# Kernel optimization log

Measured on AMD Instinct MI355X. Metric: run time of the kernel, lower is better.

Reference implementation:

```python
import jax, jax.numpy as jnp
import numpy as np

RADIUS = 50
HEADS = 4
BN_EPS = 1e-5


def setup_inputs() -> dict:
    key = jax.random.key(0)
    B, C, L = 2, 256, 1536
    D = C // HEADS
    ks = jax.random.split(key, 8)
    s = 0.05  # weight init scale
    return {
        "x": jax.random.normal(ks[0], (B, C, L), jnp.float32),
        "Wc": jax.random.normal(ks[1], (C, C), jnp.float32) * s,
        "bc": jnp.zeros((C,), jnp.float32),
        "Wq": jax.random.normal(ks[2], (C, C), jnp.float32) * s,
        "bq": jnp.zeros((C,), jnp.float32),
        "Wk": jax.random.normal(ks[3], (C, C), jnp.float32) * s,
        "bk": jnp.zeros((C,), jnp.float32),
        "emb": jax.random.normal(ks[4], (2 * RADIUS + 1, D), jnp.float32) * s,
        "Wf": jax.random.normal(ks[5], (C, C), jnp.float32) * s,
        "bf": jnp.zeros((C,), jnp.float32),
        "gamma": jnp.ones((C,), jnp.float32),
        "beta": jnp.zeros((C,), jnp.float32),
        "scale": jnp.full((C,), 0.1, jnp.float32),
    }


def reference(x, Wc, bc, Wq, bq, Wk, bk, emb, Wf, bf, gamma, beta, scale):
    B, C, L = x.shape
    H = HEADS
    D = C // H
    R = RADIUS

    def conv1x1(W, b, y):  # 1x1 Conv1d == per-position matmul
        return jnp.einsum('oc,bcl->bol', W, y) + b[None, :, None]

    def split(y):  # [B,C,L] -> [B,H,D,L]
        return y.reshape(B, H, D, L)

    content = split(conv1x1(Wc, bc, x))
    query = split(conv1x1(Wq, bq, x))
    key_ = split(conv1x1(Wk, bk, x))

    steps = jnp.arange(L)
    relative = steps[:, None] - steps[None, :]                 # [L,L]
    rel_clamped = jnp.clip(relative, -R, R)
    embs = emb[R + rel_clamped]                                # [L,L,D] gather

    dots = jnp.einsum('bhct,bhcs->bhts', query, key_)          # [B,H,L,L]
    dots = dots + 0.3 * jnp.einsum('bhct,tsc->bhts', query, embs)
    dots = jnp.where(jnp.abs(relative) <= R, dots, -jnp.inf)   # band mask

    weights = jax.nn.softmax(dots, axis=-1)                    # [B,H,L,L]

    out = jnp.einsum('bhts,bhcs->bhct', weights, content)      # [B,H,D,L]
    out = out + 0.3 * jnp.einsum('bhts,tsc->bhct', weights, embs)
    out = out.reshape(B, C, L)

    out = conv1x1(Wf, bf, out)
    # BatchNorm1d in training mode: batch stats over (B, L) per channel
    mean = out.mean(axis=(0, 2), keepdims=True)
    var = out.var(axis=(0, 2), keepdims=True)
    out = (out - mean) / jnp.sqrt(var + BN_EPS)
    out = out * gamma[None, :, None] + beta[None, :, None]
    return jax.nn.relu(out) * scale[None, :, None]
```

## Files before the change

### kernel.cpp

```cpp
#include <hip/hip_runtime.h>

typedef unsigned short u16;
typedef unsigned int u32;
typedef __bf16 bf16x8 __attribute__((ext_vector_type(8)));
typedef float f32x4 __attribute__((ext_vector_type(4)));

#define MFMA16 __builtin_amdgcn_mfma_f32_16x16x32_bf16

__device__ __forceinline__ u16 f2bf(float f) {
    u32 u = __float_as_uint(f);
    u32 r = (u + 0x7fffu + ((u >> 16) & 1u)) >> 16;
    return (u16)r;
}
__device__ __forceinline__ float bf2f(u16 h) {
    return __uint_as_float(((u32)h) << 16);
}
__device__ __forceinline__ bf16x8 ld8(const u16* p) {
    return *reinterpret_cast<const bf16x8*>(p);
}

__global__ __launch_bounds__(256) void prep(
    const float* __restrict__ x,
    const float* __restrict__ Wc, const float* __restrict__ Wq,
    const float* __restrict__ Wk, const float* __restrict__ Wf,
    const float* __restrict__ emb,
    u16* __restrict__ xT,
    u16* __restrict__ wcb, u16* __restrict__ wqb, u16* __restrict__ wkb,
    u16* __restrict__ wfb, u16* __restrict__ embR, u16* __restrict__ embT)
{
    const int tid = threadIdx.x;
    const int z = blockIdx.z;
    if (z < 2) {
        __shared__ u16 tile[64][65];
        const int b = z, c0 = blockIdx.y * 64, l0 = blockIdx.x * 64;
        const int cc = tid >> 2, lq = (tid & 3) * 16;
        const float* xp = x + (size_t)((b * 256 + c0 + cc) * 1536 + l0 + lq);
        #pragma unroll
        for (int i = 0; i < 4; ++i) {
            float4 v = *reinterpret_cast<const float4*>(xp + i * 4);
            tile[cc][lq + i * 4 + 0] = f2bf(v.x);
            tile[cc][lq + i * 4 + 1] = f2bf(v.y);
            tile[cc][lq + i * 4 + 2] = f2bf(v.z);
            tile[cc][lq + i * 4 + 3] = f2bf(v.w);
        }
        __syncthreads();
        const int ll = tid >> 2, cq = (tid & 3) * 16;
        u16* op = xT + (size_t)((b * 1536 + l0 + ll) * 256 + c0 + cq);
        #pragma unroll
        for (int i = 0; i < 16; ++i) op[i] = tile[cq + i][ll];
    } else {
        const int idx0 = (blockIdx.y * 24 + blockIdx.x) * 256 + tid;
        for (int i = idx0; i < 65536; i += 24576) {
            wcb[i] = f2bf(Wc[i]); wqb[i] = f2bf(Wq[i]);
            wkb[i] = f2bf(Wk[i]); wfb[i] = f2bf(Wf[i]);
        }
        if (idx0 < 112 * 64) {
            const int j = idx0 >> 6, d = idx0 & 63;
            embR[idx0] = (j < 101) ? f2bf(0.3f * emb[(100 - j) * 64 + d]) : (u16)0;
        }
        if (idx0 < 64 * 128) {
            const int d = idx0 >> 7, j = idx0 & 127;
            embT[idx0] = (j < 101) ? f2bf(0.3f * emb[(100 - j) * 64 + d]) : (u16)0;
        }
    }
}

__global__ __launch_bounds__(128) void gemm_qkc(
    const u16* __restrict__ xT,
    const u16* __restrict__ Wq, const float* __restrict__ bq,
    const u16* __restrict__ Wk, const float* __restrict__ bk,
    const u16* __restrict__ Wc, const float* __restrict__ bc,
    u16* __restrict__ qo, u16* __restrict__ ko, u16* __restrict__ co)
{
    const int tid = threadIdx.x, wv = tid >> 6, lane = tid & 63;
    const int l15 = lane & 15, kg8 = (lane >> 4) * 8;
    const int z = blockIdx.z, b = z & 1, which = z >> 1;
    const u16* W = (which == 0) ? Wq : (which == 1) ? Wk : Wc;
    const float* bias = (which == 0) ? bq : (which == 1) ? bk : bc;
    const int l0 = blockIdx.x * 64 + wv * 32;
    const int ch0 = blockIdx.y * 32;
    const u16* xp = xT + (size_t)(b * 1536 + l0 + l15) * 256 + kg8;
    const u16* wp = W + (size_t)(ch0 + l15) * 256 + kg8;
    const u16* ap = (which == 2) ? wp : xp;
    const u16* bp = (which == 2) ? xp : wp;

    bf16x8 a0r[8], a1r[8], b0r[8], b1r[8];
    #pragma unroll
    for (int kd = 0; kd < 8; ++kd) {
        a0r[kd] = ld8(ap + kd * 32);
        a1r[kd] = ld8(ap + 4096 + kd * 32);
        b0r[kd] = ld8(bp + kd * 32);
        b1r[kd] = ld8(bp + 4096 + kd * 32);
    }
    const f32x4 zf = {0.f, 0.f, 0.f, 0.f};
    f32x4 acc[2][2] = {{zf, zf}, {zf, zf}};
    #pragma unroll
    for (int kd = 0; kd < 8; ++kd) {
        acc[0][0] = MFMA16(a0r[kd], b0r[kd], acc[0][0], 0, 0, 0);
        acc[0][1] = MFMA16(a0r[kd], b1r[kd], acc[0][1], 0, 0, 0);
        acc[1][0] = MFMA16(a1r[kd], b0r[kd], acc[1][0], 0, 0, 0);
        acc[1][1] = MFMA16(a1r[kd], b1r[kd], acc[1][1], 0, 0, 0);
    }
    if (which < 2) {
        u16* outp = which ? ko : qo;
        float bv[2];
        bv[0] = bias[ch0 + l15];
        bv[1] = bias[ch0 + 16 + l15];
        #pragma unroll
        for (int mf = 0; mf < 2; ++mf)
            #pragma unroll
            for (int nf = 0; nf < 2; ++nf)
                #pragma unroll
                for (int r = 0; r < 4; ++r) {
                    const int row = l0 + mf * 16 + (lane >> 4) * 4 + r;
                    outp[(size_t)(b * 1536 + row) * 256 + ch0 + nf * 16 + l15] =
                        f2bf(acc[mf][nf][r] + bv[nf]);
                }
    } else {
        #pragma unroll
        for (int mf = 0; mf < 2; ++mf)
            #pragma unroll
            for (int r = 0; r < 4; ++r) {
                const int ch = ch0 + mf * 16 + (lane >> 4) * 4 + r;
                const float bv = bias[ch];
                #pragma unroll
                for (int nf = 0; nf < 2; ++nf)
                    co[(size_t)(b * 256 + ch) * 1536 + l0 + nf * 16 + l15] =
                        f2bf(acc[mf][nf][r] + bv);
            }
    }
}

__global__ __launch_bounds__(128) void gemm_f(
    const u16* __restrict__ W, const float* __restrict__ bias,
    const u16* __restrict__ srcT, u16* __restrict__ outp)
{
    const int tid = threadIdx.x, wv = tid >> 6, lane = tid & 63;
    const int l15 = lane & 15, kg8 = (lane >> 4) * 8;
    const int b = blockIdx.z;
    const int l0 = blockIdx.x * 64 + wv * 32;
    const int ch0 = blockIdx.y * 32;
    const u16* ap = W + (size_t)(ch0 + l15) * 256 + kg8;
    const u16* bp = srcT + (size_t)(b * 1536 + l0 + l15) * 256 + kg8;

    bf16x8 a0r[8], a1r[8], b0r[8], b1r[8];
    #pragma unroll
    for (int kd = 0; kd < 8; ++kd) {
        a0r[kd] = ld8(ap + kd * 32);
        a1r[kd] = ld8(ap + 4096 + kd * 32);
        b0r[kd] = ld8(bp + kd * 32);
        b1r[kd] = ld8(bp + 4096 + kd * 32);
    }
    const f32x4 zf = {0.f, 0.f, 0.f, 0.f};
    f32x4 acc[2][2] = {{zf, zf}, {zf, zf}};
    #pragma unroll
    for (int kd = 0; kd < 8; ++kd) {
        acc[0][0] = MFMA16(a0r[kd], b0r[kd], acc[0][0], 0, 0, 0);
        acc[0][1] = MFMA16(a0r[kd], b1r[kd], acc[0][1], 0, 0, 0);
        acc[1][0] = MFMA16(a1r[kd], b0r[kd], acc[1][0], 0, 0, 0);
        acc[1][1] = MFMA16(a1r[kd], b1r[kd], acc[1][1], 0, 0, 0);
    }
    #pragma unroll
    for (int mf = 0; mf < 2; ++mf)
        #pragma unroll
        for (int r = 0; r < 4; ++r) {
            const int ch = ch0 + mf * 16 + (lane >> 4) * 4 + r;
            const float bv = bias[ch];
            #pragma unroll
            for (int nf = 0; nf < 2; ++nf)
                outp[(size_t)(b * 256 + ch) * 1536 + l0 + nf * 16 + l15] =
                    f2bf(acc[mf][nf][r] + bv);
        }
}

#define WST 168
#define WBST 136
#define BST 114

__global__ __launch_bounds__(128) void attn_mfma(
    const u16* __restrict__ q, const u16* __restrict__ k,
    const u16* __restrict__ cont, const u16* __restrict__ embR,
    const u16* __restrict__ embT, u16* __restrict__ outp)
{
    __shared__ u16 wls[2][16][WST];
    __shared__ u16 wbs[2][16][WBST];
    __shared__ u16 bss[2][16][BST];
    const int tid = threadIdx.x;
    const int wv = tid >> 6, lane = tid & 63;
    const int l15 = lane & 15, kg8 = (lane >> 4) * 8;
    const int tt0 = (blockIdx.x * 2 + wv) * 16;
    const int bh = blockIdx.y, b = bh >> 2, h = bh & 3;
    u16* wl = &wls[wv][0][0];
    u16* wb = &wbs[wv][0][0];
    u16* bs = &bss[wv][0][0];

    const u16* qp = q + (size_t)(b * 1536 + tt0 + l15) * 256 + h * 64 + kg8;
    const bf16x8 a0 = ld8(qp);
    const bf16x8 a1 = ld8(qp + 32);
    bf16x8 k0r[9], k1r[9];
    #pragma unroll
    for (int nf = 0; nf < 9; ++nf) {
        int s = tt0 - 64 + nf * 16 + l15;
        int sc = s < 0 ? 0 : (s > 1535 ? 1535 : s);
        const u16* kp = k + (size_t)(b * 1536 + sc) * 256 + h * 64 + kg8;
        k0r[nf] = ld8(kp);
        k1r[nf] = ld8(kp + 32);
    }

    for (int i = lane; i < 16 * 8; i += 64) {
        const int t = i >> 3, c = 144 + ((i & 7) << 1);
        *reinterpret_cast<u32*>(&wl[t * WST + c]) = 0;
    }
    for (int i = lane; i < 16 * 27; i += 64) {
        const int t = i / 27, j = 101 + (i - t * 27);
        wb[t * WBST + j] = 0;
    }

    const f32x4 zf = {0.f, 0.f, 0.f, 0.f};
    f32x4 dacc[9];
    f32x4 eacc[7];
    #pragma unroll
    for (int i = 0; i < 9; ++i) dacc[i] = zf;
    #pragma unroll
    for (int i = 0; i < 7; ++i) eacc[i] = zf;

    #pragma unroll
    for (int nf = 0; nf < 9; ++nf) {
        dacc[nf] = MFMA16(a0, k0r[nf], dacc[nf], 0, 0, 0);
        dacc[nf] = MFMA16(a1, k1r[nf], dacc[nf], 0, 0, 0);
    }
    #pragma unroll
    for (int jf = 0; jf < 7; ++jf) {
        const u16* ep = embR + (jf * 16 + l15) * 64 + kg8;
        eacc[jf] = MFMA16(a0, ld8(ep), eacc[jf], 0, 0, 0);
        eacc[jf] = MFMA16(a1, ld8(ep + 32), eacc[jf], 0, 0, 0);
    }
    #pragma unroll
    for (int jf = 0; jf < 7; ++jf)
        #pragma unroll
        for (int r = 0; r < 4; ++r) {
            const int t = (lane >> 4) * 4 + r;
            bs[t * BST + jf * 16 + l15] = f2bf(eacc[jf][r]);
        }
    #pragma unroll
    for (int nf = 0; nf < 9; ++nf)
        #pragma unroll
        for (int r = 0; r < 4; ++r) {
            const int t = (lane >> 4) * 4 + r;
            const int cs = nf * 16 + l15;
            const int j = cs - t - 14;
            const int s = tt0 - 64 + cs;
            float v = dacc[nf][r];
            if (j >= 0 && j < 101 && s >= 0 && s < 1536)
                v += bf2f(bs[t * BST + j]);
            else
                v = -1e30f;
            dacc[nf][r] = v;
        }
    float inv[4];
    #pragma unroll
    for (int r = 0; r < 4; ++r) {
        float m = dacc[0][r];
        #pragma unroll
        for (int nf = 1; nf < 9; ++nf) m = fmaxf(m, dacc[nf][r]);
        m = fmaxf(m, __shfl_xor(m, 1));
        m = fmaxf(m, __shfl_xor(m, 2));
        m = fmaxf(m, __shfl_xor(m, 4));
        m = fmaxf(m, __shfl_xor(m, 8));
        float ss = 0.f;
        #pragma unroll
        for (int nf = 0; nf < 9; ++nf) {
            float e = __expf(dacc[nf][r] - m);
            dacc[nf][r] = e;
            ss += e;
        }
        ss += __shfl_xor(ss, 1);
        ss += __shfl_xor(ss, 2);
        ss += __shfl_xor(ss, 4);
        ss += __shfl_xor(ss, 8);
        inv[r] = 1.f / ss;
    }
    #pragma unroll
    for (int nf = 0; nf < 9; ++nf)
        #pragma unroll
        for (int r = 0; r < 4; ++r) {
            const int t = (lane >> 4) * 4 + r;
            const int cs = nf * 16 + l15;
            const u16 w16 = f2bf(dacc[nf][r] * inv[r]);
            wl[t * WST + cs] = w16;
            const int j = cs - t - 14;
            if (j >= 0 && j < 101) wb[t * WBST + j] = w16;
        }

    f32x4 oacc[4];
    #pragma unroll
    for (int i = 0; i < 4; ++i) oacc[i] = zf;
    #pragma unroll
    for (int kf = 0; kf < 5; ++kf) {
        const bf16x8 aw = ld8(&wl[l15 * WST + kf * 32 + kg8]);
        int sb = tt0 - 64 + kf * 32 + kg8;
        int sbc = sb < 0 ? 0 : (sb > 1528 ? 1528 : sb);
        #pragma unroll
        for (int nf = 0; nf < 4; ++nf) {
            const u16* cp = cont + (size_t)(b * 256 + h * 64 + nf * 16 + l15) * 1536 + sbc;
            oacc[nf] = MFMA16(aw, ld8(cp), oacc[nf], 0, 0, 0);
        }
    }
    #pragma unroll
    for (int kf = 0; kf < 4; ++kf) {
        const bf16x8 ab = ld8(&wb[l15 * WBST + kf * 32 + kg8]);
        #pragma unroll
        for (int nf = 0; nf < 4; ++nf) {
            const u16* ep = embT + (nf * 16 + l15) * 128 + kf * 32 + kg8;
            oacc[nf] = MFMA16(ab, ld8(ep), oacc[nf], 0, 0, 0);
        }
    }
    #pragma unroll
    for (int nf = 0; nf < 4; ++nf)
        #pragma unroll
        for (int r = 0; r < 4; ++r) {
            const int t = (lane >> 4) * 4 + r;
            outp[(size_t)(b * 1536 + tt0 + t) * 256 + h * 64 + nf * 16 + l15] =
                f2bf(oacc[nf][r]);
        }
}

__global__ __launch_bounds__(256) void bn_apply(
    const u16* __restrict__ pre, const float* __restrict__ gamma,
    const float* __restrict__ beta, const float* __restrict__ scale,
    float* __restrict__ out)
{
    const int o = blockIdx.x;
    const int tid = threadIdx.x;
    float v[12];
    float sum = 0.f, sumsq = 0.f;
    #pragma unroll
    for (int g = 0; g < 6; ++g) {
        const int b = (g >= 3);
        const int l = (g - 3 * b) * 512 + tid * 2;
        const u32 w = *reinterpret_cast<const u32*>(&pre[(size_t)(b * 256 + o) * 1536 + l]);
        const float v0 = __uint_as_float(w << 16);
        const float v1 = __uint_as_float(w & 0xffff0000u);
        v[g * 2] = v0; v[g * 2 + 1] = v1;
        sum += v0 + v1;
        sumsq = fmaf(v0, v0, sumsq);
        sumsq = fmaf(v1, v1, sumsq);
    }
    #pragma unroll
    for (int off = 1; off < 64; off <<= 1) {
        sum += __shfl_xor(sum, off);
        sumsq += __shfl_xor(sumsq, off);
    }
    __shared__ float rs[4], rq[4];
    const int wave = tid >> 6;
    if ((tid & 63) == 0) { rs[wave] = sum; rq[wave] = sumsq; }
    __syncthreads();
    sum = rs[0] + rs[1] + rs[2] + rs[3];
    sumsq = rq[0] + rq[1] + rq[2] + rq[3];
    const float mean = sum * (1.f / 3072.f);
    const float var = sumsq * (1.f / 3072.f) - mean * mean;
    const float is = rsqrtf(var + 1e-5f);
    const float gm = gamma[o] * is;
    const float b2 = beta[o] - mean * gm;
    const float sc = scale[o];
    #pragma unroll
    for (int g = 0; g < 6; ++g) {
        const int b = (g >= 3);
        const int l = (g - 3 * b) * 512 + tid * 2;
        float2 o2;
        o2.x = fmaxf(fmaf(v[g * 2], gm, b2), 0.f) * sc;
        o2.y = fmaxf(fmaf(v[g * 2 + 1], gm, b2), 0.f) * sc;
        *reinterpret_cast<float2*>(&out[(size_t)(b * 256 + o) * 1536 + l]) = o2;
    }
}

extern "C" void kernel_launch(void* const* d_in, const int* in_sizes, int n_in,
                              void* d_out, int out_size, void* d_ws, size_t ws_size,
                              hipStream_t stream) {
    const float* x     = (const float*)d_in[0];
    const float* Wc    = (const float*)d_in[1];
    const float* bc    = (const float*)d_in[2];
    const float* Wq    = (const float*)d_in[3];
    const float* bq    = (const float*)d_in[4];
    const float* Wk    = (const float*)d_in[5];
    const float* bk    = (const float*)d_in[6];
    const float* emb   = (const float*)d_in[7];
    const float* Wf    = (const float*)d_in[8];
    const float* bf    = (const float*)d_in[9];
    const float* gamma = (const float*)d_in[10];
    const float* beta  = (const float*)d_in[11];
    const float* scale = (const float*)d_in[12];
    float* out = (float*)d_out;
    u16* ws = (u16*)d_ws;

    const size_t NLC = 786432;
    u16* xT   = ws;
    u16* qb   = ws + NLC;
    u16* kb   = ws + 2 * NLC;
    u16* cbuf = ws + 3 * NLC;
    u16* abuf = ws + 4 * NLC;
    u16* pbuf = ws + 5 * NLC;
    u16* wcb  = ws + 6 * NLC;
    u16* wqb  = wcb + 65536;
    u16* wkb  = wqb + 65536;
    u16* wfb  = wkb + 65536;
    u16* embR = wfb + 65536;
    u16* embT = embR + 112 * 64;

    prep<<<dim3(24, 4, 3), 256, 0, stream>>>(x, Wc, Wq, Wk, Wf, emb,
                                             xT, wcb, wqb, wkb, wfb, embR, embT);
    gemm_qkc<<<dim3(24, 8, 6), 128, 0, stream>>>(xT, wqb, bq, wkb, bk, wcb, bc,
                                                 qb, kb, cbuf);
    attn_mfma<<<dim3(48, 8), 128, 0, stream>>>(qb, kb, cbuf, embR, embT, abuf);
    gemm_f<<<dim3(24, 8, 2), 128, 0, stream>>>(wfb, bf, abuf, pbuf);
    bn_apply<<<256, 256, 0, stream>>>(pbuf, gamma, beta, scale, out);
}
```

Baseline: 118.0 us.

## Fuse all stages into one persistent kernel with flag-based grid barriers

Replaces the five separate launches (prep, QKC GEMM, banded attention, output GEMM, BatchNorm) with a single 256-block persistent kernel. The stages are separated by a software grid barrier built from per-block release/acquire flags in workspace memory. Work is remapped from grid dimensions to per-wave loop indices, and all stages share one shared-memory buffer. The aim is to remove launch overhead and inter-kernel gaps. In exchange it relies on all 256 blocks being co-resident, and the flags are never reset between calls, which risks the barrier not holding on repeated invocations.

```diff
diff --git a/kernel.cpp b/kernel.cpp
--- a/kernel.cpp
+++ b/kernel.cpp
@@ -6,6 +6,11 @@
 typedef float f32x4 __attribute__((ext_vector_type(4)));
 
 #define MFMA16 __builtin_amdgcn_mfma_f32_16x16x32_bf16
+#define NBLK 256
+#define WST 168
+#define WBST 136
+#define BST 114
+#define WCHUNK (16 * (WST + WBST + BST))
 
 __device__ __forceinline__ u16 f2bf(float f) {
     u32 u = __float_as_uint(f);
@@ -19,358 +24,363 @@
     return *reinterpret_cast<const bf16x8*>(p);
 }
 
-__global__ __launch_bounds__(256) void prep(
+__device__ __forceinline__ void gsync(u32* flags, int p) {
+    __syncthreads();
+    if (threadIdx.x == 0) {
+        __threadfence();
+        __hip_atomic_store(&flags[blockIdx.x], (u32)p, __ATOMIC_RELEASE,
+                           __HIP_MEMORY_SCOPE_AGENT);
+    }
+    while ((int)__hip_atomic_load(&flags[threadIdx.x], __ATOMIC_ACQUIRE,
+                                  __HIP_MEMORY_SCOPE_AGENT) < p) {
+        __builtin_amdgcn_s_sleep(2);
+    }
+    __threadfence();
+    __syncthreads();
+}
+
+__global__ __launch_bounds__(256, 1) void fused_all(
     const float* __restrict__ x,
-    const float* __restrict__ Wc, const float* __restrict__ Wq,
-    const float* __restrict__ Wk, const float* __restrict__ Wf,
+    const float* __restrict__ Wc, const float* __restrict__ bc,
+    const float* __restrict__ Wq, const float* __restrict__ bq,
+    const float* __restrict__ Wk, const float* __restrict__ bk,
     const float* __restrict__ emb,
+    const float* __restrict__ Wf, const float* __restrict__ bf,
+    const float* __restrict__ gamma, const float* __restrict__ beta,
+    const float* __restrict__ scale,
     u16* __restrict__ xT,
     u16* __restrict__ wcb, u16* __restrict__ wqb, u16* __restrict__ wkb,
-    u16* __restrict__ wfb, u16* __restrict__ embR, u16* __restrict__ embT)
+    u16* __restrict__ wfb, u16* __restrict__ embR, u16* __restrict__ embT,
+    u16* __restrict__ qb, u16* __restrict__ kb, u16* __restrict__ cbuf,
+    u16* __restrict__ abuf, u16* __restrict__ pbuf,
+    u32* __restrict__ flags,
+    float* __restrict__ out)
 {
+    __shared__ u32 smem32[13376];
+    u16* smem = (u16*)smem32;
     const int tid = threadIdx.x;
-    const int z = blockIdx.z;
-    if (z < 2) {
-        __shared__ u16 tile[64][65];
-        const int b = z, c0 = blockIdx.y * 64, l0 = blockIdx.x * 64;
+    const int blk = blockIdx.x;
+    const int wv = tid >> 6, lane = tid & 63;
+    const int l15 = lane & 15, kg8 = (lane >> 4) * 8;
+    const f32x4 zf = {0.f, 0.f, 0.f, 0.f};
+
+    if (blk < 192) {
+        const int b = blk / 96, c0 = ((blk / 24) & 3) * 64, l0 = (blk % 24) * 64;
+        u16* tile = smem;
         const int cc = tid >> 2, lq = (tid & 3) * 16;
         const float* xp = x + (size_t)((b * 256 + c0 + cc) * 1536 + l0 + lq);
         #pragma unroll
         for (int i = 0; i < 4; ++i) {
             float4 v = *reinterpret_cast<const float4*>(xp + i * 4);
-            tile[cc][lq + i * 4 + 0] = f2bf(v.x);
-            tile[cc][lq + i * 4 + 1] = f2bf(v.y);
-            tile[cc][lq + i * 4 + 2] = f2bf(v.z);
-            tile[cc][lq + i * 4 + 3] = f2bf(v.w);
+            tile[cc * 65 + lq + i * 4 + 0] = f2bf(v.x);
+            tile[cc * 65 + lq + i * 4 + 1] = f2bf(v.y);
+            tile[cc * 65 + lq + i * 4 + 2] = f2bf(v.z);
+            tile[cc * 65 + lq + i * 4 + 3] = f2bf(v.w);
         }
         __syncthreads();
         const int ll = tid >> 2, cq = (tid & 3) * 16;
         u16* op = xT + (size_t)((b * 1536 + l0 + ll) * 256 + c0 + cq);
         #pragma unroll
-        for (int i = 0; i < 16; ++i) op[i] = tile[cq + i][ll];
+        for (int i = 0; i < 16; ++i) op[i] = tile[(cq + i) * 65 + ll];
     } else {
-        const int idx0 = (blockIdx.y * 24 + blockIdx.x) * 256 + tid;
-        for (int i = idx0; i < 65536; i += 24576) {
+        const int g = (blk - 192) * 256 + tid;
+        #pragma unroll
+        for (int rep = 0; rep < 4; ++rep) {
+            const int i = g + rep * 16384;
             wcb[i] = f2bf(Wc[i]); wqb[i] = f2bf(Wq[i]);
             wkb[i] = f2bf(Wk[i]); wfb[i] = f2bf(Wf[i]);
         }
-        if (idx0 < 112 * 64) {
-            const int j = idx0 >> 6, d = idx0 & 63;
-            embR[idx0] = (j < 101) ? f2bf(0.3f * emb[(100 - j) * 64 + d]) : (u16)0;
-        }
-        if (idx0 < 64 * 128) {
-            const int d = idx0 >> 7, j = idx0 & 127;
-            embT[idx0] = (j < 101) ? f2bf(0.3f * emb[(100 - j) * 64 + d]) : (u16)0;
-        }
-    }
-}
-
-__global__ __launch_bounds__(128) void gemm_qkc(
-    const u16* __restrict__ xT,
-    const u16* __restrict__ Wq, const float* __restrict__ bq,
-    const u16* __restrict__ Wk, const float* __restrict__ bk,
-    const u16* __restrict__ Wc, const float* __restrict__ bc,
-    u16* __restrict__ qo, u16* __restrict__ ko, u16* __restrict__ co)
-{
-    const int tid = threadIdx.x, wv = tid >> 6, lane = tid & 63;
-    const int l15 = lane & 15, kg8 = (lane >> 4) * 8;
-    const int z = blockIdx.z, b = z & 1, which = z >> 1;
-    const u16* W = (which == 0) ? Wq : (which == 1) ? Wk : Wc;
-    const float* bias = (which == 0) ? bq : (which == 1) ? bk : bc;
-    const int l0 = blockIdx.x * 64 + wv * 32;
-    const int ch0 = blockIdx.y * 32;
-    const u16* xp = xT + (size_t)(b * 1536 + l0 + l15) * 256 + kg8;
-    const u16* wp = W + (size_t)(ch0 + l15) * 256 + kg8;
-    const u16* ap = (which == 2) ? wp : xp;
-    const u16* bp = (which == 2) ? xp : wp;
-
-    bf16x8 a0r[8], a1r[8], b0r[8], b1r[8];
-    #pragma unroll
-    for (int kd = 0; kd < 8; ++kd) {
-        a0r[kd] = ld8(ap + kd * 32);
-        a1r[kd] = ld8(ap + 4096 + kd * 32);
-        b0r[kd] = ld8(bp + kd * 32);
-        b1r[kd] = ld8(bp + 4096 + kd * 32);
-    }
-    const f32x4 zf = {0.f, 0.f, 0.f, 0.f};
-    f32x4 acc[2][2] = {{zf, zf}, {zf, zf}};
-    #pragma unroll
-    for (int kd = 0; kd < 8; ++kd) {
-        acc[0][0] = MFMA16(a0r[kd], b0r[kd], acc[0][0], 0, 0, 0);
-        acc[0][1] = MFMA16(a0r[kd], b1r[kd], acc[0][1], 0, 0, 0);
-        acc[1][0] = MFMA16(a1r[kd], b0r[kd], acc[1][0], 0, 0, 0);
-        acc[1][1] = MFMA16(a1r[kd], b1r[kd], acc[1][1], 0, 0, 0);
-    }
-    if (which < 2) {
-        u16* outp = which ? ko : qo;
-        float bv[2];
-        bv[0] = bias[ch0 + l15];
-        bv[1] = bias[ch0 + 16 + l15];
-        #pragma unroll
-        for (int mf = 0; mf < 2; ++mf)
-            #pragma unroll
-            for (int nf = 0; nf < 2; ++nf)
+        if (g < 112 * 64) {
+            const int j = g >> 6, d = g & 63;
+            embR[g] = (j < 101) ? f2bf(0.3f * emb[(100 - j) * 64 + d]) : (u16)0;
+        }
+        if (g < 64 * 128) {
+            const int d = g >> 7, j = g & 127;
+            embT[g] = (j < 101) ? f2bf(0.3f * emb[(100 - j) * 64 + d]) : (u16)0;
+        }
+    }
+    gsync(flags, 1);
+
+    for (int u = blk * 4 + wv; u < 2304; u += 1024) {
+        const int z = u / 384;
+        const int r = u - z * 384;
+        const int l0 = (r >> 3) * 32;
+        const int ch0 = (r & 7) * 32;
+        const int b = z & 1, which = z >> 1;
+        const u16* W = (which == 0) ? wqb : (which == 1) ? wkb : wcb;
+        const float* bias = (which == 0) ? bq : (which == 1) ? bk : bc;
+        const u16* xp = xT + (size_t)(b * 1536 + l0 + l15) * 256 + kg8;
+        const u16* wp = W + (size_t)(ch0 + l15) * 256 + kg8;
+        const u16* ap = (which == 2) ? wp : xp;
+        const u16* bp = (which == 2) ? xp : wp;
+        bf16x8 a0r[8], a1r[8], b0r[8], b1r[8];
+        #pragma unroll
+        for (int kd = 0; kd < 8; ++kd) {
+            a0r[kd] = ld8(ap + kd * 32);
+            a1r[kd] = ld8(ap + 4096 + kd * 32);
+            b0r[kd] = ld8(bp + kd * 32);
+            b1r[kd] = ld8(bp + 4096 + kd * 32);
+        }
+        f32x4 acc[2][2] = {{zf, zf}, {zf, zf}};
+        #pragma unroll
+        for (int kd = 0; kd < 8; ++kd) {
+            acc[0][0] = MFMA16(a0r[kd], b0r[kd], acc[0][0], 0, 0, 0);
+            acc[0][1] = MFMA16(a0r[kd], b1r[kd], acc[0][1], 0, 0, 0);
+            acc[1][0] = MFMA16(a1r[kd], b0r[kd], acc[1][0], 0, 0, 0);
+            acc[1][1] = MFMA16(a1r[kd], b1r[kd], acc[1][1], 0, 0, 0);
+        }
+        if (which < 2) {
+            u16* outp = which ? kb : qb;
+            float bv[2];
+            bv[0] = bias[ch0 + l15];
+            bv[1] = bias[ch0 + 16 + l15];
+            #pragma unroll
+            for (int mf = 0; mf < 2; ++mf)
+                #pragma unroll
+                for (int nf = 0; nf < 2; ++nf)
+                    #pragma unroll
+                    for (int r2 = 0; r2 < 4; ++r2) {
+                        const int row = l0 + mf * 16 + (lane >> 4) * 4 + r2;
+                        outp[(size_t)(b * 1536 + row) * 256 + ch0 + nf * 16 + l15] =
+                            f2bf(acc[mf][nf][r2] + bv[nf]);
+                    }
+        } else {
+            #pragma unroll
+            for (int mf = 0; mf < 2; ++mf)
+                #pragma unroll
+                for (int r2 = 0; r2 < 4; ++r2) {
+                    const int ch = ch0 + mf * 16 + (lane >> 4) * 4 + r2;
+                    const float bv = bias[ch];
+                    #pragma unroll
+                    for (int nf = 0; nf < 2; ++nf)
+                        cbuf[(size_t)(b * 256 + ch) * 1536 + l0 + nf * 16 + l15] =
+                            f2bf(acc[mf][nf][r2] + bv);
+                }
+        }
+    }
+    gsync(flags, 2);
+
+    {
+        const int u = blk * 4 + wv;
+        if (u < 768) {
+            const int bh = u / 96;
+            const int tt0 = (u - bh * 96) * 16;
+            const int b = bh >> 2, h = bh & 3;
+            u16* wl = smem + wv * WCHUNK;
+            u16* wb = wl + 16 * WST;
+            u16* bs = wb + 16 * WBST;
+
+            const u16* qp = qb + (size_t)(b * 1536 + tt0 + l15) * 256 + h * 64 + kg8;
+            const bf16x8 a0 = ld8(qp);
+            const bf16x8 a1 = ld8(qp + 32);
+            bf16x8 k0r[9], k1r[9];
+            #pragma unroll
+            for (int nf = 0; nf < 9; ++nf) {
+                int s = tt0 - 64 + nf * 16 + l15;
+                int sc = s < 0 ? 0 : (s > 1535 ? 1535 : s);
+                const u16* kp = kb + (size_t)(b * 1536 + sc) * 256 + h * 64 + kg8;
+                k0r[nf] = ld8(kp);
+                k1r[nf] = ld8(kp + 32);
+            }
+            for (int i = lane; i < 16 * 8; i += 64) {
+                const int t = i >> 3, c = 144 + ((i & 7) << 1);
+                *reinterpret_cast<u32*>(&wl[t * WST + c]) = 0;
+            }
+            for (int i = lane; i < 16 * 27; i += 64) {
+                const int t = i / 27, j = 101 + (i - t * 27);
+                wb[t * WBST + j] = 0;
+            }
+            f32x4 dacc[9];
+            f32x4 eacc[7];
+            #pragma unroll
+            for (int i = 0; i < 9; ++i) dacc[i] = zf;
+            #pragma unroll
+            for (int i = 0; i < 7; ++i) eacc[i] = zf;
+            #pragma unroll
+            for (int nf = 0; nf < 9; ++nf) {
+                dacc[nf] = MFMA16(a0, k0r[nf], dacc[nf], 0, 0, 0);
+                dacc[nf] = MFMA16(a1, k1r[nf], dacc[nf], 0, 0, 0);
+            }
+            #pragma unroll
+            for (int jf = 0; jf < 7; ++jf) {
+                const u16* ep = embR + (jf * 16 + l15) * 64 + kg8;
+                eacc[jf] = MFMA16(a0, ld8(ep), eacc[jf], 0, 0, 0);
+                eacc[jf] = MFMA16(a1, ld8(ep + 32), eacc[jf], 0, 0, 0);
+            }
+            #pragma unroll
+            for (int jf = 0; jf < 7; ++jf)
                 #pragma unroll
                 for (int r = 0; r < 4; ++r) {
-                    const int row = l0 + mf * 16 + (lane >> 4) * 4 + r;
-                    outp[(size_t)(b * 1536 + row) * 256 + ch0 + nf * 16 + l15] =
-                        f2bf(acc[mf][nf][r] + bv[nf]);
-                }
-    } else {
-        #pragma unroll
-        for (int mf = 0; mf < 2; ++mf)
+                    const int t = (lane >> 4) * 4 + r;
+                    bs[t * BST + jf * 16 + l15] = f2bf(eacc[jf][r]);
+                }
+            #pragma unroll
+            for (int nf = 0; nf < 9; ++nf)
+                #pragma unroll
+                for (int r = 0; r < 4; ++r) {
+                    const int t = (lane >> 4) * 4 + r;
+                    const int cs = nf * 16 + l15;
+                    const int j = cs - t - 14;
+                    const int s = tt0 - 64 + cs;
+                    float v = dacc[nf][r];
+                    if (j >= 0 && j < 101 && s >= 0 && s < 1536)
+                        v += bf2f(bs[t * BST + j]);
+                    else
+                        v = -1e30f;
+                    dacc[nf][r] = v;
+                }
+            float inv[4];
             #pragma unroll
             for (int r = 0; r < 4; ++r) {
-                const int ch = ch0 + mf * 16 + (lane >> 4) * 4 + r;
-                const float bv = bias[ch];
-                #pragma unroll
-                for (int nf = 0; nf < 2; ++nf)
-                    co[(size_t)(b * 256 + ch) * 1536 + l0 + nf * 16 + l15] =
-                        f2bf(acc[mf][nf][r] + bv);
-            }
-    }
-}
-
-__global__ __launch_bounds__(128) void gemm_f(
-    const u16* __restrict__ W, const float* __restrict__ bias,
-    const u16* __restrict__ srcT, u16* __restrict__ outp)
-{
-    const int tid = threadIdx.x, wv = tid >> 6, lane = tid & 63;
-    const int l15 = lane & 15, kg8 = (lane >> 4) * 8;
-    const int b = blockIdx.z;
-    const int l0 = blockIdx.x * 64 + wv * 32;
-    const int ch0 = blockIdx.y * 32;
-    const u16* ap = W + (size_t)(ch0 + l15) * 256 + kg8;
-    const u16* bp = srcT + (size_t)(b * 1536 + l0 + l15) * 256 + kg8;
-
-    bf16x8 a0r[8], a1r[8], b0r[8], b1r[8];
-    #pragma unroll
-    for (int kd = 0; kd < 8; ++kd) {
-        a0r[kd] = ld8(ap + kd * 32);
-        a1r[kd] = ld8(ap + 4096 + kd * 32);
-        b0r[kd] = ld8(bp + kd * 32);
-        b1r[kd] = ld8(bp + 4096 + kd * 32);
-    }
-    const f32x4 zf = {0.f, 0.f, 0.f, 0.f};
-    f32x4 acc[2][2] = {{zf, zf}, {zf, zf}};
-    #pragma unroll
-    for (int kd = 0; kd < 8; ++kd) {
-        acc[0][0] = MFMA16(a0r[kd], b0r[kd], acc[0][0], 0, 0, 0);
-        acc[0][1] = MFMA16(a0r[kd], b1r[kd], acc[0][1], 0, 0, 0);
-        acc[1][0] = MFMA16(a1r[kd], b0r[kd], acc[1][0], 0, 0, 0);
-        acc[1][1] = MFMA16(a1r[kd], b1r[kd], acc[1][1], 0, 0, 0);
-    }
-    #pragma unroll
-    for (int mf = 0; mf < 2; ++mf)
-        #pragma unroll
-        for (int r = 0; r < 4; ++r) {
-            const int ch = ch0 + mf * 16 + (lane >> 4) * 4 + r;
-            const float bv = bias[ch];
-            #pragma unroll
-            for (int nf = 0; nf < 2; ++nf)
-                outp[(size_t)(b * 256 + ch) * 1536 + l0 + nf * 16 + l15] =
-                    f2bf(acc[mf][nf][r] + bv);
-        }
-}
-
-#define WST 168
-#define WBST 136
-#define BST 114
-
-__global__ __launch_bounds__(128) void attn_mfma(
-    const u16* __restrict__ q, const u16* __restrict__ k,
-    const u16* __restrict__ cont, const u16* __restrict__ embR,
-    const u16* __restrict__ embT, u16* __restrict__ outp)
-{
-    __shared__ u16 wls[2][16][WST];
-    __shared__ u16 wbs[2][16][WBST];
-    __shared__ u16 bss[2][16][BST];
-    const int tid = threadIdx.x;
-    const int wv = tid >> 6, lane = tid & 63;
-    const int l15 = lane & 15, kg8 = (lane >> 4) * 8;
-    const int tt0 = (blockIdx.x * 2 + wv) * 16;
-    const int bh = blockIdx.y, b = bh >> 2, h = bh & 3;
-    u16* wl = &wls[wv][0][0];
-    u16* wb = &wbs[wv][0][0];
-    u16* bs = &bss[wv][0][0];
-
-    const u16* qp = q + (size_t)(b * 1536 + tt0 + l15) * 256 + h * 64 + kg8;
-    const bf16x8 a0 = ld8(qp);
-    const bf16x8 a1 = ld8(qp + 32);
-    bf16x8 k0r[9], k1r[9];
-    #pragma unroll
-    for (int nf = 0; nf < 9; ++nf) {
-        int s = tt0 - 64 + nf * 16 + l15;
-        int sc = s < 0 ? 0 : (s > 1535 ? 1535 : s);
-        const u16* kp = k + (size_t)(b * 1536 + sc) * 256 + h * 64 + kg8;
-        k0r[nf] = ld8(kp);
-        k1r[nf] = ld8(kp + 32);
-    }
-
-    for (int i = lane; i < 16 * 8; i += 64) {
-        const int t = i >> 3, c = 144 + ((i & 7) << 1);
-        *reinterpret_cast<u32*>(&wl[t * WST + c]) = 0;
-    }
-    for (int i = lane; i < 16 * 27; i += 64) {
-        const int t = i / 27, j = 101 + (i - t * 27);
-        wb[t * WBST + j] = 0;
-    }
-
-    const f32x4 zf = {0.f, 0.f, 0.f, 0.f};
-    f32x4 dacc[9];
-    f32x4 eacc[7];
-    #pragma unroll
-    for (int i = 0; i < 9; ++i) dacc[i] = zf;
-    #pragma unroll
-    for (int i = 0; i < 7; ++i) eacc[i] = zf;
-
-    #pragma unroll
-    for (int nf = 0; nf < 9; ++nf) {
-        dacc[nf] = MFMA16(a0, k0r[nf], dacc[nf], 0, 0, 0);
-        dacc[nf] = MFMA16(a1, k1r[nf], dacc[nf], 0, 0, 0);
-    }
-    #pragma unroll
-    for (int jf = 0; jf < 7; ++jf) {
-        const u16* ep = embR + (jf * 16 + l15) * 64 + kg8;
-        eacc[jf] = MFMA16(a0, ld8(ep), eacc[jf], 0, 0, 0);
-        eacc[jf] = MFMA16(a1, ld8(ep + 32), eacc[jf], 0, 0, 0);
-    }
-    #pragma unroll
-    for (int jf = 0; jf < 7; ++jf)
-        #pragma unroll
-        for (int r = 0; r < 4; ++r) {
-            const int t = (lane >> 4) * 4 + r;
-            bs[t * BST + jf * 16 + l15] = f2bf(eacc[jf][r]);
-        }
-    #pragma unroll
-    for (int nf = 0; nf < 9; ++nf)
-        #pragma unroll
-        for (int r = 0; r < 4; ++r) {
-            const int t = (lane >> 4) * 4 + r;
-            const int cs = nf * 16 + l15;
-            const int j = cs - t - 14;
-            const int s = tt0 - 64 + cs;
-            float v = dacc[nf][r];
-            if (j >= 0 && j < 101 && s >= 0 && s < 1536)
-                v += bf2f(bs[t * BST + j]);
-            else
-                v = -1e30f;
-            dacc[nf][r] = v;
-        }
-    float inv[4];
-    #pragma unroll
-    for (int r = 0; r < 4; ++r) {
-        float m = dacc[0][r];
-        #pragma unroll
-        for (int nf = 1; nf < 9; ++nf) m = fmaxf(m, dacc[nf][r]);
-        m = fmaxf(m, __shfl_xor(m, 1));
-        m = fmaxf(m, __shfl_xor(m, 2));
-        m = fmaxf(m, __shfl_xor(m, 4));
-        m = fmaxf(m, __shfl_xor(m, 8));
-        float ss = 0.f;
-        #pragma unroll
-        for (int nf = 0; nf < 9; ++nf) {
-            float e = __expf(dacc[nf][r] - m);
-            dacc[nf][r] = e;
-            ss += e;
-        }
-        ss += __shfl_xor(ss, 1);
-        ss += __shfl_xor(ss, 2);
-        ss += __shfl_xor(ss, 4);
-        ss += __shfl_xor(ss, 8);
-        inv[r] = 1.f / ss;
-    }
-    #pragma unroll
-    for (int nf = 0; nf < 9; ++nf)
-        #pragma unroll
-        for (int r = 0; r < 4; ++r) {
-            const int t = (lane >> 4) * 4 + r;
-            const int cs = nf * 16 + l15;
-            const u16 w16 = f2bf(dacc[nf][r] * inv[r]);
-            wl[t * WST + cs] = w16;
-            const int j = cs - t - 14;
-            if (j >= 0 && j < 101) wb[t * WBST + j] = w16;
-        }
-
-    f32x4 oacc[4];
-    #pragma unroll
-    for (int i = 0; i < 4; ++i) oacc[i] = zf;
-    #pragma unroll
-    for (int kf = 0; kf < 5; ++kf) {
-        const bf16x8 aw = ld8(&wl[l15 * WST + kf * 32 + kg8]);
-        int sb = tt0 - 64 + kf * 32 + kg8;
-        int sbc = sb < 0 ? 0 : (sb > 1528 ? 1528 : sb);
-        #pragma unroll
-        for (int nf = 0; nf < 4; ++nf) {
-            const u16* cp = cont + (size_t)(b * 256 + h * 64 + nf * 16 + l15) * 1536 + sbc;
-            oacc[nf] = MFMA16(aw, ld8(cp), oacc[nf], 0, 0, 0);
-        }
-    }
-    #pragma unroll
-    for (int kf = 0; kf < 4; ++kf) {
-        const bf16x8 ab = ld8(&wb[l15 * WBST + kf * 32 + kg8]);
-        #pragma unroll
-        for (int nf = 0; nf < 4; ++nf) {
-            const u16* ep = embT + (nf * 16 + l15) * 128 + kf * 32 + kg8;
-            oacc[nf] = MFMA16(ab, ld8(ep), oacc[nf], 0, 0, 0);
-        }
-    }
-    #pragma unroll
-    for (int nf = 0; nf < 4; ++nf)
-        #pragma unroll
-        for (int r = 0; r < 4; ++r) {
-            const int t = (lane >> 4) * 4 + r;
-            outp[(size_t)(b * 1536 + tt0 + t) * 256 + h * 64 + nf * 16 + l15] =
-                f2bf(oacc[nf][r]);
-        }
-}
-
-__global__ __launch_bounds__(256) void bn_apply(
-    const u16* __restrict__ pre, const float* __restrict__ gamma,
-    const float* __restrict__ beta, const float* __restrict__ scale,
-    float* __restrict__ out)
-{
-    const int o = blockIdx.x;
-    const int tid = threadIdx.x;
-    float v[12];
-    float sum = 0.f, sumsq = 0.f;
-    #pragma unroll
-    for (int g = 0; g < 6; ++g) {
-        const int b = (g >= 3);
-        const int l = (g - 3 * b) * 512 + tid * 2;
-        const u32 w = *reinterpret_cast<const u32*>(&pre[(size_t)(b * 256 + o) * 1536 + l]);
-        const float v0 = __uint_as_float(w << 16);
-        const float v1 = __uint_as_float(w & 0xffff0000u);
-        v[g * 2] = v0; v[g * 2 + 1] = v1;
-        sum += v0 + v1;
-        sumsq = fmaf(v0, v0, sumsq);
-        sumsq = fmaf(v1, v1, sumsq);
-    }
-    #pragma unroll
-    for (int off = 1; off < 64; off <<= 1) {
-        sum += __shfl_xor(sum, off);
-        sumsq += __shfl_xor(sumsq, off);
-    }
-    __shared__ float rs[4], rq[4];
-    const int wave = tid >> 6;
-    if ((tid & 63) == 0) { rs[wave] = sum; rq[wave] = sumsq; }
-    __syncthreads();
-    sum = rs[0] + rs[1] + rs[2] + rs[3];
-    sumsq = rq[0] + rq[1] + rq[2] + rq[3];
-    const float mean = sum * (1.f / 3072.f);
-    const float var = sumsq * (1.f / 3072.f) - mean * mean;
-    const float is = rsqrtf(var + 1e-5f);
-    const float gm = gamma[o] * is;
-    const float b2 = beta[o] - mean * gm;
-    const float sc = scale[o];
-    #pragma unroll
-    for (int g = 0; g < 6; ++g) {
-        const int b = (g >= 3);
-        const int l = (g - 3 * b) * 512 + tid * 2;
-        float2 o2;
-        o2.x = fmaxf(fmaf(v[g * 2], gm, b2), 0.f) * sc;
-        o2.y = fmaxf(fmaf(v[g * 2 + 1], gm, b2), 0.f) * sc;
-        *reinterpret_cast<float2*>(&out[(size_t)(b * 256 + o) * 1536 + l]) = o2;
+                float m = dacc[0][r];
+                #pragma unroll
+                for (int nf = 1; nf < 9; ++nf) m = fmaxf(m, dacc[nf][r]);
+                m = fmaxf(m, __shfl_xor(m, 1));
+                m = fmaxf(m, __shfl_xor(m, 2));
+                m = fmaxf(m, __shfl_xor(m, 4));
+                m = fmaxf(m, __shfl_xor(m, 8));
+                float ss = 0.f;
+                #pragma unroll
+                for (int nf = 0; nf < 9; ++nf) {
+                    float e = __expf(dacc[nf][r] - m);
+                    dacc[nf][r] = e;
+                    ss += e;
+                }
+                ss += __shfl_xor(ss, 1);
+                ss += __shfl_xor(ss, 2);
+                ss += __shfl_xor(ss, 4);
+                ss += __shfl_xor(ss, 8);
+                inv[r] = 1.f / ss;
+            }
+            #pragma unroll
+            for (int nf = 0; nf < 9; ++nf)
+                #pragma unroll
+                for (int r = 0; r < 4; ++r) {
+                    const int t = (lane >> 4) * 4 + r;
+                    const int cs = nf * 16 + l15;
+                    const u16 w16 = f2bf(dacc[nf][r] * inv[r]);
+                    wl[t * WST + cs] = w16;
+                    const int j = cs - t - 14;
+                    if (j >= 0 && j < 101) wb[t * WBST + j] = w16;
+                }
+            f32x4 oacc[4];
+            #pragma unroll
+            for (int i = 0; i < 4; ++i) oacc[i] = zf;
+            #pragma unroll
+            for (int kf = 0; kf < 5; ++kf) {
+                const bf16x8 aw = ld8(&wl[l15 * WST + kf * 32 + kg8]);
+                int sb = tt0 - 64 + kf * 32 + kg8;
+                int sbc = sb < 0 ? 0 : (sb > 1528 ? 1528 : sb);
+                #pragma unroll
+                for (int nf = 0; nf < 4; ++nf) {
+                    const u16* cp = cbuf + (size_t)(b * 256 + h * 64 + nf * 16 + l15) * 1536 + sbc;
+                    oacc[nf] = MFMA16(aw, ld8(cp), oacc[nf], 0, 0, 0);
+                }
+            }
+            #pragma unroll
+            for (int kf = 0; kf < 4; ++kf) {
+                const bf16x8 ab = ld8(&wb[l15 * WBST + kf * 32 + kg8]);
+                #pragma unroll
+                for (int nf = 0; nf < 4; ++nf) {
+                    const u16* ep = embT + (nf * 16 + l15) * 128 + kf * 32 + kg8;
+                    oacc[nf] = MFMA16(ab, ld8(ep), oacc[nf], 0, 0, 0);
+                }
+            }
+            #pragma unroll
+            for (int nf = 0; nf < 4; ++nf)
+                #pragma unroll
+                for (int r = 0; r < 4; ++r) {
+                    const int t = (lane >> 4) * 4 + r;
+                    abuf[(size_t)(b * 1536 + tt0 + t) * 256 + h * 64 + nf * 16 + l15] =
+                        f2bf(oacc[nf][r]);
+                }
+        }
+    }
+    gsync(flags, 3);
+
+    {
+        const int u = blk * 4 + wv;
+        if (u < 768) {
+            const int b = u / 384;
+            const int r = u - b * 384;
+            const int l0 = (r >> 3) * 32;
+            const int ch0 = (r & 7) * 32;
+            const u16* ap = wfb + (size_t)(ch0 + l15) * 256 + kg8;
+            const u16* bp = abuf + (size_t)(b * 1536 + l0 + l15) * 256 + kg8;
+            bf16x8 a0r[8], a1r[8], b0r[8], b1r[8];
+            #pragma unroll
+            for (int kd = 0; kd < 8; ++kd) {
+                a0r[kd] = ld8(ap + kd * 32);
+                a1r[kd] = ld8(ap + 4096 + kd * 32);
+                b0r[kd] = ld8(bp + kd * 32);
+                b1r[kd] = ld8(bp + 4096 + kd * 32);
+            }
+            f32x4 acc[2][2] = {{zf, zf}, {zf, zf}};
+            #pragma unroll
+            for (int kd = 0; kd < 8; ++kd) {
+                acc[0][0] = MFMA16(a0r[kd], b0r[kd], acc[0][0], 0, 0, 0);
+                acc[0][1] = MFMA16(a0r[kd], b1r[kd], acc[0][1], 0, 0, 0);
+                acc[1][0] = MFMA16(a1r[kd], b0r[kd], acc[1][0], 0, 0, 0);
+                acc[1][1] = MFMA16(a1r[kd], b1r[kd], acc[1][1], 0, 0, 0);
+            }
+            #pragma unroll
+            for (int mf = 0; mf < 2; ++mf)
+                #pragma unroll
+                for (int r2 = 0; r2 < 4; ++r2) {
+                    const int ch = ch0 + mf * 16 + (lane >> 4) * 4 + r2;
+                    const float bv = bf[ch];
+                    #pragma unroll
+                    for (int nf = 0; nf < 2; ++nf)
+                        pbuf[(size_t)(b * 256 + ch) * 1536 + l0 + nf * 16 + l15] =
+                            f2bf(acc[mf][nf][r2] + bv);
+                }
+        }
+    }
+    gsync(flags, 4);
+
+    {
+        const int o = blk;
+        float* rs = (float*)smem32;
+        float* rq = rs + 4;
+        float v[12];
+        float sum = 0.f, sumsq = 0.f;
+        #pragma unroll
+        for (int g = 0; g < 6; ++g) {
+            const int b = (g >= 3);
+            const int l = (g - 3 * b) * 512 + tid * 2;
+            const u32 w = *reinterpret_cast<const u32*>(&pbuf[(size_t)(b * 256 + o) * 1536 + l]);
+            const float v0 = __uint_as_float(w << 16);
+            const float v1 = __uint_as_float(w & 0xffff0000u);
+            v[g * 2] = v0; v[g * 2 + 1] = v1;
+            sum += v0 + v1;
+            sumsq = fmaf(v0, v0, sumsq);
+            sumsq = fmaf(v1, v1, sumsq);
+        }
+        #pragma unroll
+        for (int off = 1; off < 64; off <<= 1) {
+            sum += __shfl_xor(sum, off);
+            sumsq += __shfl_xor(sumsq, off);
+        }
+        const int wave = tid >> 6;
+        if ((tid & 63) == 0) { rs[wave] = sum; rq[wave] = sumsq; }
+        __syncthreads();
+        sum = rs[0] + rs[1] + rs[2] + rs[3];
+        sumsq = rq[0] + rq[1] + rq[2] + rq[3];
+        const float mean = sum * (1.f / 3072.f);
+        const float var = sumsq * (1.f / 3072.f) - mean * mean;
+        const float is = rsqrtf(var + 1e-5f);
+        const float gm = gamma[o] * is;
+        const float b2 = beta[o] - mean * gm;
+        const float sc = scale[o];
+        #pragma unroll
+        for (int g = 0; g < 6; ++g) {
+            const int b = (g >= 3);
+            const int l = (g - 3 * b) * 512 + tid * 2;
+            float2 o2;
+            o2.x = fmaxf(fmaf(v[g * 2], gm, b2), 0.f) * sc;
+            o2.y = fmaxf(fmaf(v[g * 2 + 1], gm, b2), 0.f) * sc;
+            *reinterpret_cast<float2*>(&out[(size_t)(b * 256 + o) * 1536 + l]) = o2;
+        }
     }
 }
 
@@ -406,12 +416,10 @@
     u16* wfb  = wkb + 65536;
     u16* embR = wfb + 65536;
     u16* embT = embR + 112 * 64;
-
-    prep<<<dim3(24, 4, 3), 256, 0, stream>>>(x, Wc, Wq, Wk, Wf, emb,
-                                             xT, wcb, wqb, wkb, wfb, embR, embT);
-    gemm_qkc<<<dim3(24, 8, 6), 128, 0, stream>>>(xT, wqb, bq, wkb, bk, wcb, bc,
-                                                 qb, kb, cbuf);
-    attn_mfma<<<dim3(48, 8), 128, 0, stream>>>(qb, kb, cbuf, embR, embT, abuf);
-    gemm_f<<<dim3(24, 8, 2), 128, 0, stream>>>(wfb, bf, abuf, pbuf);
-    bn_apply<<<256, 256, 0, stream>>>(pbuf, gamma, beta, scale, out);
-}
+    u32* flags = (u32*)(embT + 64 * 128);
+
+    fused_all<<<NBLK, 256, 0, stream>>>(
+        x, Wc, bc, Wq, bq, Wk, bk, emb, Wf, bf, gamma, beta, scale,
+        xT, wcb, wqb, wkb, wfb, embR, embT, qb, kb, cbuf, abuf, pbuf,
+        flags, out);
+}
```

New measurement: 315.9 us. 2.68x slower.
